# Kernel tuning notes

Measured on AMD Instinct MI355X. Metric: run time of the kernel, lower is better.

Reference implementation:

```python
import jax, jax.numpy as jnp
import numpy as np
import math

B, N_TOK, C, H = 8, 1024, 384, 6
K, S, P = 3, 2, 1
OUT_C, HID = 384, 4 * 384
EPS = 1e-5
NEG_INF = float('-inf')


def _build_conv_mask(num_token, k, s, p):
    """Replicates ConvAttentionMask (include_cls_token=True). Returns (mask[(N+2),(N+2)], idx[(W,k^2)] with -1 for padding)."""
    I = int(math.sqrt(num_token))
    ref = np.arange(num_token).reshape(I, I)
    ref = np.pad(ref, ((0, p), (0, p)), constant_values=-1)
    cent = np.arange(k // 2 - p, I - k // 2 + p, s)
    cc = np.stack(np.meshgrid(cent, cent, indexing='ij'), -1).reshape(-1, 1, 2)  # cartesian_prod order
    ke = np.arange(-(k // 2), k // 2 + 1)
    kc = np.stack(np.meshgrid(ke, ke, indexing='ij'), -1).reshape(1, -1, 2)
    coords = cc + kc  # (W, k^2, 2); negative coords wrap like torch fancy indexing -> hit -1 padding
    idx = ref[coords[..., 0], coords[..., 1]]  # (W, k^2)
    mask = np.full((num_token, num_token), NEG_INF, np.float32)
    for w in idx:
        v = w[w >= 0]
        mask[np.ix_(v, v)] = 1.0
    idx = idx + (idx >= 0).astype(np.int32)  # shift for cls token; -1 stays -1
    mask = np.pad(mask, ((1, 0), (1, 0)), constant_values=1.0)  # cls row/col
    mask = np.pad(mask, ((0, 1), (0, 1)), constant_values=0.0)  # extra zero-padded token
    return mask, idx

MASK_NP, IDX_NP = _build_conv_mask(N_TOK, K, S, P)
W_WIN = IDX_NP.shape[0]
# torch negative index -1 on a length-(N_TOK+1) tensor -> wrap to last token
IDX_FLAT = np.where(IDX_NP < 0, IDX_NP + N_TOK + 1, IDX_NP).reshape(-1)


def _ln(x, w, b):
    mu = jnp.mean(x, -1, keepdims=True)
    var = jnp.mean(jnp.square(x - mu), -1, keepdims=True)
    return (x - mu) * jax.lax.rsqrt(var + EPS) * w + b


def setup_inputs() -> dict:
    key = jax.random.key(0)
    ks = jax.random.split(key, 8)
    sd = 0.02
    return {
        'x': jax.random.normal(ks[0], (B, N_TOK + 1, C), jnp.float32),
        'norm1_w': jnp.ones((C,), jnp.float32), 'norm1_b': jnp.zeros((C,), jnp.float32),
        'qkv_w': sd * jax.random.normal(ks[1], (3 * C, C), jnp.float32),
        'proj_w': sd * jax.random.normal(ks[2], (C, C), jnp.float32),
        'proj_b': jnp.zeros((C,), jnp.float32),
        'norm2_w': jnp.ones((C,), jnp.float32), 'norm2_b': jnp.zeros((C,), jnp.float32),
        'pool_w': sd * jax.random.normal(ks[3], (C, K * K * C), jnp.float32),
        'pool_b': jnp.zeros((C,), jnp.float32),
        'norm3_w': jnp.ones((C,), jnp.float32), 'norm3_b': jnp.zeros((C,), jnp.float32),
        'fc1_w': sd * jax.random.normal(ks[4], (HID, C), jnp.float32),
        'fc1_b': jnp.zeros((HID,), jnp.float32),
        'fc2_w': sd * jax.random.normal(ks[5], (OUT_C, HID), jnp.float32),
        'fc2_b': jnp.zeros((OUT_C,), jnp.float32),
    }


def reference(x, norm1_w, norm1_b, qkv_w, proj_w, proj_b, norm2_w, norm2_b,
              pool_w, pool_b, norm3_w, norm3_b, fc1_w, fc1_b, fc2_w, fc2_b):
    mask = jnp.asarray(MASK_NP)  # (N_TOK+2, N_TOK+2), values in {-inf, 0, 1}
    Bv, N, Cv = x.shape
    d = Cv // H
    h = _ln(x, norm1_w, norm1_b)
    h = jnp.pad(h, ((0, 0), (0, 1), (0, 0)))  # append zero token -> (B, N+1, C)
    M = N + 1
    # attention (scale = num_heads**-0.5 as in the source, qkv has no bias)
    qkv = (h @ qkv_w.T).reshape(Bv, M, 3, H, d).transpose(2, 0, 3, 1, 4)
    q, k, v = qkv[0], qkv[1], qkv[2]
    scores = jnp.einsum('bhqd,bhkd->bhqk', q, k) * (H ** -0.5)
    # multiplicative mask {-inf,0,1}: keep where 1, zero where 0, -inf where -inf (intended semantics)
    scores = jnp.where(mask == 1.0, scores, jnp.where(mask == 0.0, 0.0, NEG_INF))
    probs = jax.nn.softmax(scores, axis=-1)
    attn = jnp.einsum('bhqk,bhkd->bhqd', probs, v).transpose(0, 2, 1, 3).reshape(Bv, M, Cv)
    attn = attn @ proj_w.T + proj_b
    h = h + attn
    h = h[:, :-1, :]  # drop padded token -> (B, N, C)
    h = _ln(h, norm2_w, norm2_b)
    # conv-style pooling: gather k^2 tokens per window, project
    gathered = h[:, IDX_FLAT, :].reshape(Bv, W_WIN, K * K * Cv)
    tok = gathered @ pool_w.T + pool_b  # (B, W, C)
    h = jnp.concatenate([h[:, :1, :], tok], axis=1)  # prepend cls -> (B, W+1, C)
    h = _ln(h, norm3_w, norm3_b)
    h = jax.nn.gelu(h @ fc1_w.T + fc1_b, approximate=False)
    return h @ fc2_w.T + fc2_b  # (B, W+1, OUT_C)
```

## Files before the change

### kernel.cpp

```cpp
#include <hip/hip_runtime.h>


typedef unsigned short u16;
typedef unsigned int u32;
typedef short s16x8 __attribute__((ext_vector_type(8)));
typedef float f32x4 __attribute__((ext_vector_type(4)));

__device__ __forceinline__ float b2f(u16 u) {
    return __uint_as_float(((u32)u) << 16);
}
__device__ __forceinline__ u16 f2b(float f) {
    u32 u = __float_as_uint(f);
    return (u16)((u + 0x7FFFu + ((u >> 16) & 1u)) >> 16);
}
__device__ __forceinline__ void gload16(const void* g, void* l) {
    __builtin_amdgcn_global_load_lds(
        (const __attribute__((address_space(1))) void*)g,
        (__attribute__((address_space(3))) void*)l, 16, 0, 0);
}
__device__ __forceinline__ float wave_sum(float v) {
#pragma unroll
    for (int o = 32; o > 0; o >>= 1) v += __shfl_xor(v, o, 64);
    return v;
}
__device__ __forceinline__ float wave_max(float v) {
#pragma unroll
    for (int o = 32; o > 0; o >>= 1) v = fmaxf(v, __shfl_xor(v, o, 64));
    return v;
}
__device__ __forceinline__ float half_sum(float v) {
#pragma unroll
    for (int o = 16; o > 0; o >>= 1) v += __shfl_xor(v, o, 64);
    return v;
}
__device__ __forceinline__ float half_max(float v) {
#pragma unroll
    for (int o = 16; o > 0; o >>= 1) v = fmaxf(v, __shfl_xor(v, o, 64));
    return v;
}
__device__ __forceinline__ float dot8(const float* qsh, int d0, uint4 u) {
    return qsh[d0 + 0] * b2f((u16)(u.x)) + qsh[d0 + 1] * b2f((u16)(u.x >> 16)) +
           qsh[d0 + 2] * b2f((u16)(u.y)) + qsh[d0 + 3] * b2f((u16)(u.y >> 16)) +
           qsh[d0 + 4] * b2f((u16)(u.z)) + qsh[d0 + 5] * b2f((u16)(u.z >> 16)) +
           qsh[d0 + 6] * b2f((u16)(u.w)) + qsh[d0 + 7] * b2f((u16)(u.w >> 16));
}

#define CCH 384
#define SCALE 0.40824829046386302f
#define NEG_BIG (-1e30f)

#define W_QKV 0
#define W_PROJ 442368
#define W_POOL 589824
#define W_FC1 1916928
#define W_FC2 2506752
#define W_TOTAL 3096576

__device__ __forceinline__ void ln_from_f32(const float* in, const float* w,
                                            const float* bb, u16* out,
                                            int lane) {
    float v[6];
    float s = 0.f, ss = 0.f;
#pragma unroll
    for (int i = 0; i < 6; i++) {
        v[i] = in[lane + 64 * i];
        s += v[i];
        ss += v[i] * v[i];
    }
    s = wave_sum(s);
    ss = wave_sum(ss);
    float mu = s * (1.f / 384.f);
    float var = ss * (1.f / 384.f) - mu * mu;
    float inv = rsqrtf(var + 1e-5f);
#pragma unroll
    for (int i = 0; i < 6; i++) {
        int c = lane + 64 * i;
        out[c] = f2b((v[i] - mu) * inv * w[c] + bb[c]);
    }
}
__device__ __forceinline__ void ln_from_b16(const u16* in, const float* w,
                                            const float* bb, u16* out,
                                            int lane) {
    float v[6];
    float s = 0.f, ss = 0.f;
#pragma unroll
    for (int i = 0; i < 6; i++) {
        v[i] = b2f(in[lane + 64 * i]);
        s += v[i];
        ss += v[i] * v[i];
    }
    s = wave_sum(s);
    ss = wave_sum(ss);
    float mu = s * (1.f / 384.f);
    float var = ss * (1.f / 384.f) - mu * mu;
    float inv = rsqrtf(var + 1e-5f);
#pragma unroll
    for (int i = 0; i < 6; i++) {
        int c = lane + 64 * i;
        out[c] = f2b((v[i] - mu) * inv * w[c] + bb[c]);
    }
}

#define PRO_LN 2052
#define PRO_CVT 1512
#define PRO_ZERO 771
__global__ __launch_bounds__(256) void prologue(
    const float* __restrict__ x, const float* __restrict__ n1w,
    const float* __restrict__ n1b, u16* __restrict__ h1,
    const float* __restrict__ qkv_w, const float* __restrict__ proj_w,
    const float* __restrict__ pool_w, const float* __restrict__ fc1_w,
    const float* __restrict__ fc2_w, u16* __restrict__ wb,
    float* __restrict__ dout) {
    int bid = blockIdx.x, tid = threadIdx.x;
    if (bid < PRO_LN) {
        int wv = tid >> 6, lane = tid & 63;
        int row = bid * 4 + wv;
        int t = row % 1026, b = row / 1026;
        u16* out = h1 + (size_t)row * CCH;
        if (t == 1025) {
#pragma unroll
            for (int i = 0; i < 6; i++) out[lane + 64 * i] = 0;
            return;
        }
        ln_from_f32(x + ((size_t)b * 1025 + t) * CCH, n1w, n1b, out, lane);
    } else if (bid < PRO_LN + PRO_CVT) {
        size_t off = ((size_t)(bid - PRO_LN) * 256 + tid) * 8;
        if (off >= W_TOTAL) return;
        const float* src;
        size_t base;
        if (off < W_PROJ)       { src = qkv_w;  base = W_QKV; }
        else if (off < W_POOL)  { src = proj_w; base = W_PROJ; }
        else if (off < W_FC1)   { src = pool_w; base = W_POOL; }
        else if (off < W_FC2)   { src = fc1_w;  base = W_FC1; }
        else                    { src = fc2_w;  base = W_FC2; }
        size_t rel = off - base;
        float4 a = *(const float4*)(src + rel);
        float4 b = *(const float4*)(src + rel + 4);
        uint4 o;
        o.x = (u32)f2b(a.x) | ((u32)f2b(a.y) << 16);
        o.y = (u32)f2b(a.z) | ((u32)f2b(a.w) << 16);
        o.z = (u32)f2b(b.x) | ((u32)f2b(b.y) << 16);
        o.w = (u32)f2b(b.z) | ((u32)f2b(b.w) << 16);
        *(uint4*)(wb + off) = o;
    } else {
        size_t idx = ((size_t)(bid - PRO_LN - PRO_CVT) * 256 + tid) * 4;
        *(float4*)(dout + idx) = make_float4(0.f, 0.f, 0.f, 0.f);
    }
}

#define MID_LN 2050
#define MID_ZERO 768
__global__ __launch_bounds__(256) void midk(u16* __restrict__ h,
                                            const float* __restrict__ n2w,
                                            const float* __restrict__ n2b,
                                            float* __restrict__ tokf) {
    int bid = blockIdx.x, tid = threadIdx.x;
    if (bid < MID_LN) {
        int wv = tid >> 6, lane = tid & 63;
        int row = bid * 4 + wv;
        int b = row / 1025, t = row % 1025;
        u16* p = h + ((size_t)b * 1026 + t) * CCH;
        ln_from_b16(p, n2w, n2b, p, lane);
    } else {
        size_t idx = ((size_t)(bid - MID_LN) * 256 + tid) * 4;
        *(float4*)(tokf + idx) = make_float4(0.f, 0.f, 0.f, 0.f);
    }
}

__global__ __launch_bounds__(64) void ln3_concat(const u16* __restrict__ h2,
                                                 const float* __restrict__ tokf,
                                                 const float* __restrict__ w,
                                                 const float* __restrict__ bb,
                                                 u16* __restrict__ h3) {
    int row = blockIdx.x;
    int b = row / 257, t = row % 257;
    int lane = threadIdx.x;
    u16* out = h3 + (size_t)row * CCH;
    if (t == 0) {
        ln_from_b16(h2 + (size_t)b * 1026 * CCH, w, bb, out, lane);
    } else {
        ln_from_f32(tokf + ((size_t)b * 256 + (t - 1)) * CCH, w, bb, out, lane);
    }
}

template <int TN, bool GATHER, int SPLITK, bool BIAS, bool GELU_ACT, bool RES,
          bool ATOMIC>
__global__ __launch_bounds__(256) void gemm_mf(const u16* __restrict__ A,
                                               int lda,
                                               const u16* __restrict__ Bwb,
                                               const float* __restrict__ bias,
                                               const u16* __restrict__ Res,
                                               void* __restrict__ Yv, int M,
                                               int N, int K) {
    __shared__ u16 Asl[128 * 32];
    __shared__ u16 Bsl[TN * 32];
    const int tid = threadIdx.x;
    const int wave = tid >> 6, lane = tid & 63;
    const int quad = lane >> 4, l15 = lane & 15;
    const int wvu = __builtin_amdgcn_readfirstlane(wave);
    const int m0 = blockIdx.y * 128, n0 = blockIdx.x * TN;
    const int kp = (SPLITK > 1) ? blockIdx.z : 0;
    const int KS = K / SPLITK;
    const int kbase = kp * KS;
    const int srow = tid >> 2;
    const int sseg = (tid & 3) ^ (srow & 3);

    f32x4 acc[2][TN / 16];
#pragma unroll
    for (int i = 0; i < 2; i++)
#pragma unroll
        for (int j = 0; j < TN / 16; j++) acc[i][j] = (f32x4){0.f, 0.f, 0.f, 0.f};

    for (int kt = 0; kt < KS; kt += 32) {
        const int kk = kbase + kt;
        const int kf = kk + sseg * 8;
#pragma unroll
        for (int L = 0; L < 2; L++) {
            int row = L * 64 + srow;
            const u16* src;
            if (GATHER) {
                int m = m0 + row;
                int b = m >> 8, w = m & 255;
                int j = kf / 384, rem = kf - j * 384;
                int pr = 2 * (w >> 4) + j / 3 - 1;
                int pc = 2 * (w & 15) + j % 3 - 1;
                int tok = (pr >= 0 && pr < 32 && pc >= 0 && pc < 32)
                              ? (32 * pr + pc + 1)
                              : 1024;
                src = A + ((size_t)b * 1026 + tok) * 384 + rem;
            } else {
                int m = m0 + row;
                if (m >= M) m = M - 1;
                src = A + (size_t)m * lda + kf;
            }
            gload16(src, &Asl[(size_t)(L * 256 + wvu * 64) * 8]);
        }
#pragma unroll
        for (int L = 0; L < TN / 64; L++) {
            int row = L * 64 + srow;
            gload16(Bwb + (size_t)(n0 + row) * K + kf,
                    &Bsl[(size_t)(L * 256 + wvu * 64) * 8]);
        }
        __syncthreads();
        s16x8 afr[2], bfr[TN / 16];
        const int rslot = (quad ^ (l15 & 3)) * 8;
#pragma unroll
        for (int ms = 0; ms < 2; ms++)
            afr[ms] =
                *(const s16x8*)(&Asl[(wave * 32 + ms * 16 + l15) * 32 + rslot]);
#pragma unroll
        for (int ns = 0; ns < TN / 16; ns++)
            bfr[ns] = *(const s16x8*)(&Bsl[(ns * 16 + l15) * 32 + rslot]);
#pragma unroll
        for (int ms = 0; ms < 2; ms++)
#pragma unroll
            for (int ns = 0; ns < TN / 16; ns++)
                acc[ms][ns] = __builtin_amdgcn_mfma_f32_16x16x32_bf16(
                    afr[ms], bfr[ns], acc[ms][ns], 0, 0, 0);
        __syncthreads();
    }
#pragma unroll
    for (int ms = 0; ms < 2; ms++) {
#pragma unroll
        for (int ns = 0; ns < TN / 16; ns++) {
            int n = n0 + ns * 16 + l15;
#pragma unroll
            for (int i = 0; i < 4; i++) {
                int m = m0 + wave * 32 + ms * 16 + quad * 4 + i;
                if (m >= M) continue;
                float v = acc[ms][ns][i];
                if (BIAS && (SPLITK == 1 || kp == 0)) v += bias[n];
                if (RES) v += b2f(Res[(size_t)m * N + n]);
                if (GELU_ACT) v = 0.5f * v * (1.f + erff(v * 0.70710678118f));
                if (ATOMIC)
                    atomicAdd((float*)Yv + (size_t)m * N + n, v);
                else
                    ((u16*)Yv)[(size_t)m * N + n] = f2b(v);
            }
        }
    }
}

__global__ __launch_bounds__(64) void attn_patch(u16* __restrict__ qkv) {
    int bid = blockIdx.x;
    int idx = bid & 511;
    int hb = bid >> 9;
    int h = hb % 6, b = hb / 6;
    int lane = threadIdx.x;
    int hl = lane >> 5, l5 = lane & 31;
    int p0 = idx * 2;
    int p = p0 | hl;
    int r = p >> 5, c = p & 31;
    int rlo, rhi, clo, chi;
    if (r & 1) { rlo = (r - 2 < 0) ? 0 : r - 2; rhi = (r + 2 > 31) ? 31 : r + 2; }
    else       { rlo = (r - 1 < 0) ? 0 : r - 1; rhi = (r + 1 > 31) ? 31 : r + 1; }
    if (c & 1) { clo = (c - 2 < 0) ? 0 : c - 2; chi = (c + 2 > 31) ? 31 : c + 2; }
    else       { clo = (c - 1 < 0) ? 0 : c - 1; chi = (c + 1 > 31) ? 31 : c + 1; }
    int nr = rhi - rlo + 1, nc = chi - clo + 1;
    int nk = nr * nc + 1;
    int tok = 0;
    if (l5 >= 1 && l5 < nk) {
        int jj = l5 - 1;
        tok = 1 + ((rlo + jj / nc) << 5) + (clo + jj % nc);
    }
    u16* base = qkv + (size_t)b * 1026 * 1152 + h * 64;
    __shared__ float qsh[2][64];
    qsh[0][lane] = b2f(base[(size_t)(1 + p0) * 1152 + lane]);
    qsh[1][lane] = b2f(base[(size_t)(2 + p0) * 1152 + lane]);
    __syncthreads();
    float sc = NEG_BIG;
    if (l5 < nk) {
        const u16* krow = base + (size_t)tok * 1152 + 384;
        float acc = 0.f;
#pragma unroll
        for (int d0 = 0; d0 < 64; d0 += 8)
            acc += dot8(qsh[hl], d0, *(const uint4*)(krow + d0));
        sc = acc * SCALE;
    }
    float mx = fmaxf(half_max(sc), 0.f);
    float pe = (l5 < nk) ? expf(sc - mx) : 0.f;
    float Z = half_sum(pe) + expf(-mx);
    float o0 = 0.f, o1 = 0.f;
#pragma unroll
    for (int j = 0; j < 26; j++) {
        int t = __shfl(tok, (hl << 5) | j, 64);
        float wj = __shfl(pe, (hl << 5) | j, 64);
        u32 vv = *(const u32*)(base + (size_t)t * 1152 + 768 + 2 * l5);
        o0 += wj * b2f((u16)vv);
        o1 += wj * b2f((u16)(vv >> 16));
    }
    float zi = 1.f / Z;
    u32 packed = (u32)f2b(o0 * zi) | ((u32)f2b(o1 * zi) << 16);
    *(u32*)(base + (size_t)(1 + p) * 1152 + 2 * l5) = packed;
}

__global__ __launch_bounds__(1024) void attn_cls(u16* __restrict__ qkv) {
    int h = blockIdx.x % 6, b = blockIdx.x / 6;
    u16* base = qkv + (size_t)b * 1026 * 1152 + h * 64;
    int tid = threadIdx.x, lane = tid & 63, wv = tid >> 6;
    __shared__ float sc[1026];
    __shared__ float qsh[64];
    __shared__ float redmax[16], redsum[16];
    __shared__ float pv[16][64];
    if (tid < 64) qsh[tid] = b2f(base[tid]);
    __syncthreads();
    for (int key = tid; key < 1026; key += 1024) {
        const u16* krow = base + (size_t)key * 1152 + 384;
        float acc = 0.f;
#pragma unroll
        for (int d0 = 0; d0 < 64; d0 += 8)
            acc += dot8(qsh, d0, *(const uint4*)(krow + d0));
        sc[key] = acc * SCALE;
    }
    __syncthreads();
    float lm = NEG_BIG;
    for (int key = tid; key < 1026; key += 1024) lm = fmaxf(lm, sc[key]);
    lm = wave_max(lm);
    if (lane == 0) redmax[wv] = lm;
    __syncthreads();
    float mx = NEG_BIG;
#pragma unroll
    for (int i = 0; i < 16; i++) mx = fmaxf(mx, redmax[i]);
    float lsum = 0.f;
    for (int key = tid; key < 1026; key += 1024) {
        float e = expf(sc[key] - mx);
        sc[key] = e;
        lsum += e;
    }
    lsum = wave_sum(lsum);
    if (lane == 0) redsum[wv] = lsum;
    __syncthreads();
    float Z = 0.f;
#pragma unroll
    for (int i = 0; i < 16; i++) Z += redsum[i];
    float acc = 0.f;
#pragma unroll
    for (int t = 0; t < 65; t++) {
        int key = wv + 16 * t;
        bool ok = key < 1026;
        int kc = ok ? key : 1025;
        float p = ok ? sc[kc] : 0.f;
        acc += p * b2f(base[(size_t)kc * 1152 + 768 + lane]);
    }
    pv[wv][lane] = acc;
    __syncthreads();
    if (tid < 64) {
        float s = 0.f;
#pragma unroll
        for (int w2 = 0; w2 < 16; w2++) s += pv[w2][tid];
        base[tid] = f2b(s / Z);
        base[(size_t)1025 * 1152 + tid] = 0;
    }
}

extern "C" void kernel_launch(void* const* d_in, const int* in_sizes, int n_in,
                              void* d_out, int out_size, void* d_ws,
                              size_t ws_size, hipStream_t stream) {
    const float* x      = (const float*)d_in[0];
    const float* n1w    = (const float*)d_in[1];
    const float* n1b    = (const float*)d_in[2];
    const float* qkv_w  = (const float*)d_in[3];
    const float* proj_w = (const float*)d_in[4];
    const float* proj_b = (const float*)d_in[5];
    const float* n2w    = (const float*)d_in[6];
    const float* n2b    = (const float*)d_in[7];
    const float* pool_w = (const float*)d_in[8];
    const float* pool_b = (const float*)d_in[9];
    const float* n3w    = (const float*)d_in[10];
    const float* n3b    = (const float*)d_in[11];
    const float* fc1_w  = (const float*)d_in[12];
    const float* fc1_b  = (const float*)d_in[13];
    const float* fc2_w  = (const float*)d_in[14];
    const float* fc2_b  = (const float*)d_in[15];

    u16* ws = (u16*)d_ws;
    u16* h1    = ws;
    u16* qkvb  = ws + 3151872;
    u16* wb    = ws + 12607488;
    float* tokf = (float*)qkvb;
    u16* h3    = qkvb + 1572864;
    u16* mlp1  = qkvb + 2362368;

    prologue<<<PRO_LN + PRO_CVT + PRO_ZERO, 256, 0, stream>>>(
        x, n1w, n1b, h1, qkv_w, proj_w, pool_w, fc1_w, fc2_w, wb,
        (float*)d_out);
    gemm_mf<128, false, 1, false, false, false, false>
        <<<dim3(1152 / 128, 65), 256, 0, stream>>>(h1, 384, wb + W_QKV,
                                                   nullptr, nullptr, qkvb,
                                                   8208, 1152, 384);
    attn_patch<<<8 * 6 * 512, 64, 0, stream>>>(qkvb);
    attn_cls<<<8 * 6, 1024, 0, stream>>>(qkvb);
    gemm_mf<64, false, 1, true, false, true, false>
        <<<dim3(384 / 64, 65), 256, 0, stream>>>(qkvb, 1152, wb + W_PROJ,
                                                 proj_b, h1, h1, 8208, 384,
                                                 384);
    midk<<<MID_LN + MID_ZERO, 256, 0, stream>>>(h1, n2w, n2b, tokf);
    gemm_mf<64, true, 4, true, false, false, true>
        <<<dim3(384 / 64, 16, 4), 256, 0, stream>>>(h1, 384, wb + W_POOL,
                                                    pool_b, nullptr, tokf,
                                                    2048, 384, 3456);
    ln3_concat<<<8 * 257, 64, 0, stream>>>(h1, tokf, n3w, n3b, h3);
    gemm_mf<64, false, 1, true, true, false, false>
        <<<dim3(1536 / 64, 17), 256, 0, stream>>>(h3, 384, wb + W_FC1, fc1_b,
                                                  nullptr, mlp1, 2056, 1536,
                                                  384);
    gemm_mf<64, false, 4, true, false, false, true>
        <<<dim3(384 / 64, 17, 4), 256, 0, stream>>>(mlp1, 1536, wb + W_FC2,
                                                    fc2_b, nullptr, d_out,
                                                    2056, 384, 1536);
}
```

Measured before the change: 264.2 us.

## Double-buffer GEMM LDS tiles and change swizzle to reduce bank conflicts

The MFMA GEMM now keeps two LDS buffers for the A and B tiles and issues the global-to-LDS loads for the next k-step before computing on the current one. This is meant to overlap memory latency with the MFMA work and drops one barrier per iteration. The LDS swizzle also changes to XOR with (row ^ row>>2) so that fragment reads spread across more banks. In exchange the kernel uses twice the LDS, which may lower occupancy. There is also some risk from relying on the barrier ordering of the async global_load_lds.

```diff
diff --git a/kernel.cpp b/kernel.cpp
--- a/kernel.cpp
+++ b/kernel.cpp
@@ -192,8 +192,8 @@
                                                const u16* __restrict__ Res,
                                                void* __restrict__ Yv, int M,
                                                int N, int K) {
-    __shared__ u16 Asl[128 * 32];
-    __shared__ u16 Bsl[TN * 32];
+    __shared__ u16 Asl[2][128 * 32];
+    __shared__ u16 Bsl[2][TN * 32];
     const int tid = threadIdx.x;
     const int wave = tid >> 6, lane = tid & 63;
     const int quad = lane >> 4, l15 = lane & 15;
@@ -203,7 +203,7 @@
     const int KS = K / SPLITK;
     const int kbase = kp * KS;
     const int srow = tid >> 2;
-    const int sseg = (tid & 3) ^ (srow & 3);
+    const int sseg = (tid & 3) ^ ((srow ^ (srow >> 2)) & 3);
 
     f32x4 acc[2][TN / 16];
 #pragma unroll
@@ -211,8 +211,7 @@
 #pragma unroll
         for (int j = 0; j < TN / 16; j++) acc[i][j] = (f32x4){0.f, 0.f, 0.f, 0.f};
 
-    for (int kt = 0; kt < KS; kt += 32) {
-        const int kk = kbase + kt;
+    auto stage = [&](int buf, int kk) {
         const int kf = kk + sseg * 8;
 #pragma unroll
         for (int L = 0; L < 2; L++) {
@@ -233,31 +232,45 @@
                 if (m >= M) m = M - 1;
                 src = A + (size_t)m * lda + kf;
             }
-            gload16(src, &Asl[(size_t)(L * 256 + wvu * 64) * 8]);
+            gload16(src, &Asl[buf][(size_t)(L * 256 + wvu * 64) * 8]);
         }
 #pragma unroll
         for (int L = 0; L < TN / 64; L++) {
             int row = L * 64 + srow;
             gload16(Bwb + (size_t)(n0 + row) * K + kf,
-                    &Bsl[(size_t)(L * 256 + wvu * 64) * 8]);
-        }
-        __syncthreads();
+                    &Bsl[buf][(size_t)(L * 256 + wvu * 64) * 8]);
+        }
+    };
+
+    int cur = 0;
+    stage(0, kbase);
+    __syncthreads();
+    for (int kt = 0; kt < KS; kt += 32) {
+        const bool more = (kt + 32 < KS);
+        if (more) stage(cur ^ 1, kbase + kt + 32);
         s16x8 afr[2], bfr[TN / 16];
-        const int rslot = (quad ^ (l15 & 3)) * 8;
-#pragma unroll
-        for (int ms = 0; ms < 2; ms++)
-            afr[ms] =
-                *(const s16x8*)(&Asl[(wave * 32 + ms * 16 + l15) * 32 + rslot]);
-#pragma unroll
-        for (int ns = 0; ns < TN / 16; ns++)
-            bfr[ns] = *(const s16x8*)(&Bsl[(ns * 16 + l15) * 32 + rslot]);
+#pragma unroll
+        for (int ms = 0; ms < 2; ms++) {
+            int ar = wave * 32 + ms * 16 + l15;
+            int slot = quad ^ ((ar ^ (ar >> 2)) & 3);
+            afr[ms] = *(const s16x8*)(&Asl[cur][ar * 32 + slot * 8]);
+        }
+#pragma unroll
+        for (int ns = 0; ns < TN / 16; ns++) {
+            int br = ns * 16 + l15;
+            int slot = quad ^ ((br ^ (br >> 2)) & 3);
+            bfr[ns] = *(const s16x8*)(&Bsl[cur][br * 32 + slot * 8]);
+        }
 #pragma unroll
         for (int ms = 0; ms < 2; ms++)
 #pragma unroll
             for (int ns = 0; ns < TN / 16; ns++)
                 acc[ms][ns] = __builtin_amdgcn_mfma_f32_16x16x32_bf16(
                     afr[ms], bfr[ns], acc[ms][ns], 0, 0, 0);
-        __syncthreads();
+        if (more) {
+            __syncthreads();
+            cur ^= 1;
+        }
     }
 #pragma unroll
     for (int ms = 0; ms < 2; ms++) {
```

After: 285.0 us. +7.9%, slower.
